# Kernel tuning notes

Hardware: AMD Instinct MI355X
Metric: run time of the kernel (lower is better)

Reference implementation:

```python
import jax, jax.numpy as jnp
import numpy as np

TOP_K = 2

def setup_inputs() -> dict:
    key = jax.random.key(0)
    k0, k1, k2, k3 = jax.random.split(key, 4)
    B, S, H, I, E = 2, 2048, 1024, 1408, 8
    hidden_states = jax.random.normal(k0, (B, S, H), dtype=jnp.float32)
    router_weight = jax.random.normal(k1, (E, H), dtype=jnp.float32) * 0.02
    gate_up_proj = jax.random.normal(k2, (E, 2 * I, H), dtype=jnp.float32) * 0.02
    down_proj = jax.random.normal(k3, (E, H, I), dtype=jnp.float32) * 0.02
    return {
        "hidden_states": hidden_states,
        "router_weight": router_weight,
        "gate_up_proj": gate_up_proj,
        "down_proj": down_proj,
    }

def reference(hidden_states, router_weight, gate_up_proj, down_proj):
    B, S, H = hidden_states.shape
    E = router_weight.shape[0]
    x = hidden_states.reshape(-1, H)                       # [T, H]
    T = x.shape[0]
    # Router: logits -> float32 softmax -> top-k (matches torch: topk on probs)
    logits = x @ router_weight.T                           # [T, E]
    probs = jax.nn.softmax(logits.astype(jnp.float32), axis=-1)
    topw, topi = jax.lax.top_k(probs, TOP_K)               # [T, K]
    topw = topw.astype(x.dtype)
    # Per-token combine weights over experts (zero for non-selected experts).
    combine = jnp.zeros((T, E), dtype=x.dtype)
    combine = combine.at[jnp.arange(T)[:, None], topi].set(topw)  # [T, E]
    # Dense grouped expert compute (same math as gather-GEMM-scatter loop:
    # tokens not routed to expert e get combine weight 0).
    gu = jnp.einsum('th,eoh->teo', x, gate_up_proj)        # [T, E, 2I]
    g, u = jnp.split(gu, 2, axis=-1)                       # [T, E, I] each
    h = jax.nn.silu(g) * u                                 # [T, E, I]
    y = jnp.einsum('tei,ehi->teh', h, down_proj)           # [T, E, H]
    out = jnp.einsum('teh,te->th', y, combine)             # [T, H]
    return out.reshape(B, S, H)
```

## Files before the change

kernel.cpp:

```cpp
#include <hip/hip_runtime.h>
#include <math.h>

#define NTOK 4096
#define HDIM 1024
#define NEXP 8
#define IDIM 1408
#define TWO_I 2816
#define TM 256
#define TK 64
#define NRB 40
#define ROWCAP (NRB * 256)

typedef _Float16 f16x8 __attribute__((ext_vector_type(8)));
typedef float f32x4 __attribute__((ext_vector_type(4)));

typedef __attribute__((address_space(1))) const unsigned int gu32;
typedef __attribute__((address_space(3))) unsigned int lu32;
__device__ __forceinline__ void async16(const void* g, void* l) {
  __builtin_amdgcn_global_load_lds((gu32*)g, (lu32*)l, 16, 0, 0);
}

__device__ __forceinline__ void seg_prefix(const int* __restrict__ counts, int* aof) {
  int o = 0; aof[0] = 0;
#pragma unroll
  for (int i = 0; i < 8; i++) { o += (counts[i] + 255) & ~255; aof[i + 1] = o; }
}

extern "C" __global__ void moe_init(int* counts, int* cursor, int* tok) {
  int i = blockIdx.x * 256 + threadIdx.x;
  if (i < NEXP) { counts[i] = 0; cursor[i] = 0; }
  if (i < ROWCAP) tok[i] = -1;
}

#define NG8 (NEXP * TWO_I * HDIM / 8)
#define ND8 (NEXP * HDIM * IDIM / 8)
extern "C" __global__ void moe_cvtw(const float* __restrict__ gup, const float* __restrict__ dp,
                                    _Float16* __restrict__ guph, _Float16* __restrict__ dph) {
  int i = blockIdx.x * 256 + threadIdx.x;
  const float4* s; uint4* d; size_t idx;
  if (i < NG8) { s = (const float4*)gup; d = (uint4*)guph; idx = i; }
  else if (i < NG8 + ND8) { s = (const float4*)dp; d = (uint4*)dph; idx = i - NG8; }
  else return;
  float4 a = s[idx * 2], b = s[idx * 2 + 1];
  union { _Float16 h[8]; uint4 u; } p;
  p.h[0] = (_Float16)a.x; p.h[1] = (_Float16)a.y; p.h[2] = (_Float16)a.z; p.h[3] = (_Float16)a.w;
  p.h[4] = (_Float16)b.x; p.h[5] = (_Float16)b.y; p.h[6] = (_Float16)b.z; p.h[7] = (_Float16)b.w;
  d[idx] = p.u;
}

extern "C" __global__ void moe_router(const float* __restrict__ x,
                                      const float* __restrict__ rw,
                                      int* __restrict__ topi,
                                      float* __restrict__ topw,
                                      _Float16* __restrict__ xh) {
  int w = threadIdx.x >> 6, lane = threadIdx.x & 63;
  int t = blockIdx.x * 4 + w;
  const float4* xp = (const float4*)(x + (size_t)t * HDIM);
  const float4* rp = (const float4*)rw;
  float acc[NEXP];
#pragma unroll
  for (int e = 0; e < NEXP; e++) acc[e] = 0.f;
#pragma unroll
  for (int i = 0; i < HDIM / 256; i++) {
    float4 xv = xp[i * 64 + lane];
    union { _Float16 h[4]; uint2 u; } pk;
    pk.h[0] = (_Float16)xv.x; pk.h[1] = (_Float16)xv.y;
    pk.h[2] = (_Float16)xv.z; pk.h[3] = (_Float16)xv.w;
    *(uint2*)(xh + (size_t)t * HDIM + i * 256 + lane * 4) = pk.u;
#pragma unroll
    for (int e = 0; e < NEXP; e++) {
      float4 rv = rp[e * 256 + i * 64 + lane];
      acc[e] += xv.x * rv.x + xv.y * rv.y + xv.z * rv.z + xv.w * rv.w;
    }
  }
#pragma unroll
  for (int e = 0; e < NEXP; e++) {
#pragma unroll
    for (int off = 32; off > 0; off >>= 1) acc[e] += __shfl_down(acc[e], off);
  }
  if (lane == 0) {
    float m = acc[0];
    for (int e = 1; e < NEXP; e++) m = fmaxf(m, acc[e]);
    float p[NEXP], s = 0.f;
    for (int e = 0; e < NEXP; e++) { p[e] = __expf(acc[e] - m); s += p[e]; }
    float inv = 1.f / s;
    int i0 = 0; float b0 = p[0];
    for (int e = 1; e < NEXP; e++) if (p[e] > b0) { b0 = p[e]; i0 = e; }
    int i1 = -1; float b1 = -1.f;
    for (int e = 0; e < NEXP; e++) if (e != i0 && p[e] > b1) { b1 = p[e]; i1 = e; }
    topi[t * 2] = i0; topi[t * 2 + 1] = i1;
    topw[t * 2] = b0 * inv; topw[t * 2 + 1] = b1 * inv;
  }
}

extern "C" __global__ void moe_count(const int* __restrict__ topi, int* __restrict__ counts) {
  __shared__ int cnt[NEXP];
  if (threadIdx.x < NEXP) cnt[threadIdx.x] = 0;
  __syncthreads();
  int t = blockIdx.x * 256 + threadIdx.x;
  atomicAdd(&cnt[topi[t * 2]], 1);
  atomicAdd(&cnt[topi[t * 2 + 1]], 1);
  __syncthreads();
  if (threadIdx.x < NEXP) atomicAdd(&counts[threadIdx.x], cnt[threadIdx.x]);
}

extern "C" __global__ void moe_scatter(const int* __restrict__ topi, const float* __restrict__ topw,
                                       const int* __restrict__ counts, int* __restrict__ cursor,
                                       int* __restrict__ tok, float* __restrict__ wrow,
                                       int* __restrict__ rows) {
  __shared__ int cnt[NEXP];
  __shared__ int base[NEXP];
  int aof[9]; seg_prefix(counts, aof);
  int tid = threadIdx.x;
  if (tid < NEXP) cnt[tid] = 0;
  __syncthreads();
  int t = blockIdx.x * 256 + tid;
  int e0 = topi[t * 2], e1 = topi[t * 2 + 1];
  int r0 = atomicAdd(&cnt[e0], 1);
  int r1 = atomicAdd(&cnt[e1], 1);
  __syncthreads();
  if (tid < NEXP) base[tid] = atomicAdd(&cursor[tid], cnt[tid]);
  __syncthreads();
  int row0 = aof[e0] + base[e0] + r0;
  int row1 = aof[e1] + base[e1] + r1;
  tok[row0] = t; wrow[row0] = topw[t * 2];     rows[t * 2]     = row0;
  tok[row1] = t; wrow[row1] = topw[t * 2 + 1]; rows[t * 2 + 1] = row1;
}


#define WAITVM(n) asm volatile("s_waitcnt vmcnt(" #n ")" ::: "memory")
#define BAR() __builtin_amdgcn_s_barrier()
#define PRIO(x) __builtin_amdgcn_s_setprio(x)

#define LDV(off) (*(const f16x8*)((const char*)smem + (uint32_t)(off)))

#define RD_A(grp, BO) { \
  _Pragma("unroll") for (int m_ = 0; m_ < 4; m_++) { \
    va[m_][0] = LDV(sA0 + (BO) + ((grp)*4 + m_)*2048); \
    va[m_][1] = LDV(sA1 + (BO) + ((grp)*4 + m_)*2048); } }

#define RD_B(VB, nb, BO) { \
  _Pragma("unroll") for (int n_ = 0; n_ < 2; n_++) { \
    VB[n_][0] = LDV(sB0 + (BO) + ((nb)*2 + n_)*2048); \
    VB[n_][1] = LDV(sB1 + (BO) + ((nb)*2 + n_)*2048); } }

#define MM(qa, qb, VB) { \
  _Pragma("unroll") for (int k_ = 0; k_ < 2; k_++) \
  _Pragma("unroll") for (int m_ = 0; m_ < 4; m_++) \
  _Pragma("unroll") for (int n_ = 0; n_ < 2; n_++) \
    acc[(qa)*4 + m_][(qb)*2 + n_] = __builtin_amdgcn_mfma_f32_16x16x32_f16( \
        va[m_][k_], VB[n_][k_], acc[(qa)*4 + m_][(qb)*2 + n_], 0, 0, 0); }

#define STG4(P, bf, r0, kt) { \
  async16(P[0][0] + (kt)*TK, smem + ((bf)*4 + (r0))*8192 + wv*512); \
  async16(P[0][1] + (kt)*TK, smem + ((bf)*4 + (r0))*8192 + 4096 + wv*512); \
  async16(P[1][0] + (kt)*TK, smem + ((bf)*4 + (r0) + 1)*8192 + wv*512); \
  async16(P[1][1] + (kt)*TK, smem + ((bf)*4 + (r0) + 1)*8192 + 4096 + wv*512); }
#define STAGE_A(bf, kt) STG4(pA, bf, 0, kt)
#define STAGE_B(bf, kt) STG4(pB, bf, 2, kt)

#define GEMM_CORE(NIT) { \
  STAGE_B(0, 0); STAGE_A(0, 0); \
  STAGE_B(1, 1); STAGE_A(1, 1); \
  WAITVM(8); BAR(); \
  _Pragma("unroll 1") \
  for (int it = 0; it < (NIT); ++it) { \
    const int nl = (it + 1 < (NIT)); \
    const int kt2 = 2*it + 2, kt3 = 2*it + 3; \
     RD_B(vb0, 0, 0); RD_A(0, 0); BAR(); PRIO(1); MM(0,0,vb0); PRIO(0); BAR(); \
     RD_B(vb1, 1, 0); BAR(); PRIO(1); MM(0,1,vb1); PRIO(0); BAR(); \
     RD_A(1, 0); if (nl) STAGE_B(0, kt2); BAR(); PRIO(1); MM(1,0,vb0); PRIO(0); BAR(); \
     if (nl) { STAGE_A(0, kt2); } PRIO(1); MM(1,1,vb1); PRIO(0); \
              if (nl) { WAITVM(8); } else { WAITVM(0); } BAR(); \
     RD_B(vb0, 0, 65536); RD_A(0, 65536); BAR(); PRIO(1); MM(0,0,vb0); PRIO(0); BAR(); \
     RD_B(vb1, 1, 65536); BAR(); PRIO(1); MM(0,1,vb1); PRIO(0); BAR(); \
     RD_A(1, 65536); if (nl) STAGE_B(1, kt3); BAR(); PRIO(1); MM(1,0,vb0); PRIO(0); BAR(); \
     if (nl) { STAGE_A(1, kt3); } PRIO(1); MM(1,1,vb1); PRIO(0); \
              if (nl) { WAITVM(8); } BAR(); \
  } \
  asm volatile("" ::: "memory"); }

#define GEMM_SETUP() \
  const int tid = threadIdx.x; \
  const int lane = tid & 63, wv = tid >> 6; \
  const int wm = wv >> 2, wn = wv & 3; \
  const int quad = lane >> 4, l15 = lane & 15; \
  const int srow = tid >> 3; \
  const int kc = ((tid & 7) ^ (srow & 7)) << 3; \
  const uint32_t c0 = (uint32_t)((quad * 16) ^ ((l15 & 7) << 4)); \
  const uint32_t c1 = c0 ^ 64; \
  const uint32_t sA0 = wm * 16384 + l15 * 128 + c0; \
  const uint32_t sA1 = wm * 16384 + l15 * 128 + c1; \
  const uint32_t sB0 = (2 + (wn >> 1)) * 16384 + ((wn & 1) * 64 + l15) * 128 + c0; \
  const uint32_t sB1 = (2 + (wn >> 1)) * 16384 + ((wn & 1) * 64 + l15) * 128 + c1; \
  f32x4 acc[8][4]; \
  _Pragma("unroll") for (int m = 0; m < 8; m++) \
  _Pragma("unroll") for (int n = 0; n < 4; n++) acc[m][n] = (f32x4){0.f, 0.f, 0.f, 0.f}; \
  f16x8 va[4][2], vb0[2][2], vb1[2][2];

extern "C" __global__ __launch_bounds__(512, 2) void moe_gemm1(
    const _Float16* __restrict__ xh, const _Float16* __restrict__ guph,
    const int* __restrict__ counts, const int* __restrict__ tok,
    _Float16* __restrict__ hbuf) {
  __shared__ __align__(128) _Float16 smem[65536];
  int aof[9]; seg_prefix(counts, aof);
  const int fid = blockIdx.x;
  const int g = fid & 7, t7 = fid >> 3;
  const int j = t7 / 5, r5 = t7 - j * 5;
  const int rb = g + 8 * r5;
  const int row0 = rb * TM;
  if (row0 >= aof[8]) return;
  int e = 0;
#pragma unroll
  for (int i = 0; i < 8; i++) if (row0 >= aof[i]) e = i;

  GEMM_SETUP();

  const _Float16* pA[2][2]; const _Float16* pB[2][2];
#pragma unroll
  for (int h = 0; h < 2; h++)
#pragma unroll
    for (int q = 0; q < 2; q++) {
      int tk = tok[row0 + h * 128 + q * 64 + srow];
      tk = tk < 0 ? 0 : tk;
      pA[h][q] = xh + (size_t)tk * HDIM + kc;
    }
  const _Float16* eb = guph + (size_t)e * TWO_I * HDIM;
#pragma unroll
  for (int q = 0; q < 2; q++) {
    pB[0][q] = eb + (size_t)(j * 128 + q * 64 + srow) * HDIM + kc;
    pB[1][q] = eb + (size_t)(IDIM + j * 128 + q * 64 + srow) * HDIM + kc;
  }

  GEMM_CORE(HDIM / (2 * TK))

  if (wn >= 2) {
#pragma unroll
    for (int mf = 0; mf < 8; mf++)
#pragma unroll
      for (int nf = 0; nf < 4; nf++)
#pragma unroll
        for (int r2 = 0; r2 < 4; r2++)
          smem[(wm * 128 + mf * 16 + quad * 4 + r2) * 132 + (wn - 2) * 64 + nf * 16 + l15] =
              (_Float16)acc[mf][nf][r2];
  }
  __syncthreads();
  if (wn < 2) {
#pragma unroll
    for (int mf = 0; mf < 8; mf++) {
#pragma unroll
      for (int r2 = 0; r2 < 4; r2++) {
        const int rl = wm * 128 + mf * 16 + quad * 4 + r2;
        _Float16* orow = hbuf + (size_t)(row0 + rl) * IDIM + j * 128 + wn * 64;
#pragma unroll
        for (int nf = 0; nf < 4; nf++) {
          float gg = acc[mf][nf][r2];
          float uu = (float)smem[rl * 132 + wn * 64 + nf * 16 + l15];
          float hh = gg / (1.f + __expf(-gg)) * uu;
          orow[nf * 16 + l15] = (_Float16)hh;
        }
      }
    }
  }
}

extern "C" __global__ __launch_bounds__(512, 2) void moe_gemm2(
    const _Float16* __restrict__ hbuf, const _Float16* __restrict__ dph,
    const int* __restrict__ counts, const float* __restrict__ wrow,
    _Float16* __restrict__ yh) {
  __shared__ __align__(128) _Float16 smem[65536];
  int aof[9]; seg_prefix(counts, aof);
  const int fid = blockIdx.x;
  const int g = fid & 7, t7 = fid >> 3;
  const int cb = t7 / 5, r5 = t7 - cb * 5;
  const int rb = g + 8 * r5;
  const int row0 = rb * TM;
  if (row0 >= aof[8]) return;
  int e = 0;
#pragma unroll
  for (int i = 0; i < 8; i++) if (row0 >= aof[i]) e = i;

  GEMM_SETUP();

  const _Float16* pA[2][2]; const _Float16* pB[2][2];
#pragma unroll
  for (int h = 0; h < 2; h++)
#pragma unroll
    for (int q = 0; q < 2; q++)
      pA[h][q] = hbuf + (size_t)(row0 + h * 128 + q * 64 + srow) * IDIM + kc;
  const _Float16* eb = dph + (size_t)e * HDIM * IDIM;
#pragma unroll
  for (int h = 0; h < 2; h++)
#pragma unroll
    for (int q = 0; q < 2; q++)
      pB[h][q] = eb + (size_t)(cb * 256 + h * 128 + q * 64 + srow) * IDIM + kc;

  GEMM_CORE(IDIM / (2 * TK))

#pragma unroll
  for (int mf = 0; mf < 8; mf++) {
#pragma unroll
    for (int r2 = 0; r2 < 4; r2++) {
      const int row = row0 + wm * 128 + mf * 16 + quad * 4 + r2;
      const float wgt = wrow[row];
      _Float16* orow = yh + (size_t)row * HDIM + cb * 256 + wn * 64;
#pragma unroll
      for (int nf = 0; nf < 4; nf++)
        orow[nf * 16 + l15] = (_Float16)(acc[mf][nf][r2] * wgt);
    }
  }
}

extern "C" __global__ void moe_combine(const _Float16* __restrict__ yh,
                                       const int* __restrict__ rows,
                                       float* __restrict__ out) {
  int i = blockIdx.x * 256 + threadIdx.x;
  int t = i >> 7, c8 = i & 127;
  int rA = rows[t * 2], rB = rows[t * 2 + 1];
  union { uint4 u; _Float16 h[8]; } pa, pb;
  pa.u = ((const uint4*)(yh + (size_t)rA * HDIM))[c8];
  pb.u = ((const uint4*)(yh + (size_t)rB * HDIM))[c8];
  float4 o0, o1;
  o0.x = (float)pa.h[0] + (float)pb.h[0]; o0.y = (float)pa.h[1] + (float)pb.h[1];
  o0.z = (float)pa.h[2] + (float)pb.h[2]; o0.w = (float)pa.h[3] + (float)pb.h[3];
  o1.x = (float)pa.h[4] + (float)pb.h[4]; o1.y = (float)pa.h[5] + (float)pb.h[5];
  o1.z = (float)pa.h[6] + (float)pb.h[6]; o1.w = (float)pa.h[7] + (float)pb.h[7];
  ((float4*)out)[(size_t)i * 2] = o0;
  ((float4*)out)[(size_t)i * 2 + 1] = o1;
}

extern "C" void kernel_launch(void* const* d_in, const int* in_sizes, int n_in,
                              void* d_out, int out_size, void* d_ws, size_t ws_size,
                              hipStream_t stream) {
  const float* x   = (const float*)d_in[0];
  const float* rw  = (const float*)d_in[1];
  const float* gup = (const float*)d_in[2];
  const float* dp  = (const float*)d_in[3];
  float* out = (float*)d_out;

  char* ws = (char*)d_ws;
  int*   counts = (int*)ws;
  int*   cursor = (int*)(ws + 64);
  int*   topi   = (int*)(ws + 4096);
  float* topw   = (float*)(ws + 36864);
  int*   tok    = (int*)(ws + 69632);
  float* wrow   = (float*)(ws + 110592);
  int*   rows   = (int*)(ws + 151552);
  _Float16* xh   = (_Float16*)(ws + 184320);
  _Float16* guph = (_Float16*)(ws + 8572928);
  _Float16* dph  = (_Float16*)(ws + 54710272);
  _Float16* hbuf = (_Float16*)(ws + 77778944);
  _Float16* yh   = (_Float16*)(ws + 8572928);

  moe_init<<<(ROWCAP + 255) / 256, 256, 0, stream>>>(counts, cursor, tok);
  moe_router<<<NTOK / 4, 256, 0, stream>>>(x, rw, topi, topw, xh);
  moe_count<<<NTOK / 256, 256, 0, stream>>>(topi, counts);
  moe_scatter<<<NTOK / 256, 256, 0, stream>>>(topi, topw, counts, cursor, tok, wrow, rows);
  moe_cvtw<<<(NG8 + ND8 + 255) / 256, 256, 0, stream>>>(gup, dp, guph, dph);
  moe_gemm1<<<8 * 11 * 5, 512, 0, stream>>>(xh, guph, counts, tok, hbuf);
  moe_gemm2<<<8 * 4 * 5, 512, 0, stream>>>(hbuf, dph, counts, wrow, yh);
  moe_combine<<<NTOK * HDIM / 8 / 256, 256, 0, stream>>>(yh, rows, out);
}
```

Before: 329.3 us.

## Simplify GEMM main loop to one LDS read phase and full MFMA block per k-tile

Replaces the four-quadrant interleaved schedule (partial A/B fragment reads, MFMA quarters, and barriers between each) with a simpler loop per K tile. Each iteration reads all A and B fragments, waits on LDS, issues one barrier, stages the tile two steps ahead, then runs all 64 MFMAs. This cuts barrier count and scheduling overhead, but holds more fragment registers at once (va[8][2], vb[4][2]). It also loses the overlap between LDS reads and MFMA work, which may expose LDS latency or hurt occupancy under the 512x2 launch bounds.

```diff
diff --git a/kernel.cpp b/kernel.cpp
--- a/kernel.cpp
+++ b/kernel.cpp
@@ -131,52 +131,47 @@
 #define WAITVM(n) asm volatile("s_waitcnt vmcnt(" #n ")" ::: "memory")
 #define BAR() __builtin_amdgcn_s_barrier()
 #define PRIO(x) __builtin_amdgcn_s_setprio(x)
+#define SCHEDB() __builtin_amdgcn_sched_barrier(0)
 
 #define LDV(off) (*(const f16x8*)((const char*)smem + (uint32_t)(off)))
 
-#define RD_A(grp, BO) { \
-  _Pragma("unroll") for (int m_ = 0; m_ < 4; m_++) { \
-    va[m_][0] = LDV(sA0 + (BO) + ((grp)*4 + m_)*2048); \
-    va[m_][1] = LDV(sA1 + (BO) + ((grp)*4 + m_)*2048); } }
-
-#define RD_B(VB, nb, BO) { \
-  _Pragma("unroll") for (int n_ = 0; n_ < 2; n_++) { \
-    VB[n_][0] = LDV(sB0 + (BO) + ((nb)*2 + n_)*2048); \
-    VB[n_][1] = LDV(sB1 + (BO) + ((nb)*2 + n_)*2048); } }
-
-#define MM(qa, qb, VB) { \
+#define RD_ALL(BO) { \
+  _Pragma("unroll") for (int m_ = 0; m_ < 8; m_++) { \
+    va[m_][0] = LDV(sA0 + (BO) + m_*2048); \
+    va[m_][1] = LDV(sA1 + (BO) + m_*2048); } \
+  _Pragma("unroll") for (int n_ = 0; n_ < 4; n_++) { \
+    vb[n_][0] = LDV(sB0 + (BO) + n_*2048); \
+    vb[n_][1] = LDV(sB1 + (BO) + n_*2048); } }
+
+#define MM_ALL() { \
   _Pragma("unroll") for (int k_ = 0; k_ < 2; k_++) \
-  _Pragma("unroll") for (int m_ = 0; m_ < 4; m_++) \
-  _Pragma("unroll") for (int n_ = 0; n_ < 2; n_++) \
-    acc[(qa)*4 + m_][(qb)*2 + n_] = __builtin_amdgcn_mfma_f32_16x16x32_f16( \
-        va[m_][k_], VB[n_][k_], acc[(qa)*4 + m_][(qb)*2 + n_], 0, 0, 0); }
+  _Pragma("unroll") for (int m_ = 0; m_ < 8; m_++) \
+  _Pragma("unroll") for (int n_ = 0; n_ < 4; n_++) \
+    acc[m_][n_] = __builtin_amdgcn_mfma_f32_16x16x32_f16( \
+        va[m_][k_], vb[n_][k_], acc[m_][n_], 0, 0, 0); }
 
 #define STG4(P, bf, r0, kt) { \
   async16(P[0][0] + (kt)*TK, smem + ((bf)*4 + (r0))*8192 + wv*512); \
   async16(P[0][1] + (kt)*TK, smem + ((bf)*4 + (r0))*8192 + 4096 + wv*512); \
   async16(P[1][0] + (kt)*TK, smem + ((bf)*4 + (r0) + 1)*8192 + wv*512); \
   async16(P[1][1] + (kt)*TK, smem + ((bf)*4 + (r0) + 1)*8192 + 4096 + wv*512); }
-#define STAGE_A(bf, kt) STG4(pA, bf, 0, kt)
-#define STAGE_B(bf, kt) STG4(pB, bf, 2, kt)
+#define STAGE_T(bf, kt) { STG4(pB, bf, 2, kt); STG4(pA, bf, 0, kt); }
 
 #define GEMM_CORE(NIT) { \
-  STAGE_B(0, 0); STAGE_A(0, 0); \
-  STAGE_B(1, 1); STAGE_A(1, 1); \
+  STAGE_T(0, 0); STAGE_T(1, 1); \
   WAITVM(8); BAR(); \
   _Pragma("unroll 1") \
-  for (int it = 0; it < (NIT); ++it) { \
-    const int nl = (it + 1 < (NIT)); \
-    const int kt2 = 2*it + 2, kt3 = 2*it + 3; \
-     RD_B(vb0, 0, 0); RD_A(0, 0); BAR(); PRIO(1); MM(0,0,vb0); PRIO(0); BAR(); \
-     RD_B(vb1, 1, 0); BAR(); PRIO(1); MM(0,1,vb1); PRIO(0); BAR(); \
-     RD_A(1, 0); if (nl) STAGE_B(0, kt2); BAR(); PRIO(1); MM(1,0,vb0); PRIO(0); BAR(); \
-     if (nl) { STAGE_A(0, kt2); } PRIO(1); MM(1,1,vb1); PRIO(0); \
-              if (nl) { WAITVM(8); } else { WAITVM(0); } BAR(); \
-     RD_B(vb0, 0, 65536); RD_A(0, 65536); BAR(); PRIO(1); MM(0,0,vb0); PRIO(0); BAR(); \
-     RD_B(vb1, 1, 65536); BAR(); PRIO(1); MM(0,1,vb1); PRIO(0); BAR(); \
-     RD_A(1, 65536); if (nl) STAGE_B(1, kt3); BAR(); PRIO(1); MM(1,0,vb0); PRIO(0); BAR(); \
-     if (nl) { STAGE_A(1, kt3); } PRIO(1); MM(1,1,vb1); PRIO(0); \
-              if (nl) { WAITVM(8); } BAR(); \
+  for (int kt = 0; kt < (NIT); ++kt) { \
+    const uint32_t BO = (kt & 1) ? 65536u : 0u; \
+    RD_ALL(BO); \
+    asm volatile("s_waitcnt lgkmcnt(0)" ::: "memory"); \
+    SCHEDB(); \
+    BAR(); \
+    SCHEDB(); \
+    if (kt + 2 < (NIT)) { STAGE_T((kt & 1), kt + 2); } \
+    PRIO(1); MM_ALL(); PRIO(0); \
+    if (kt + 2 < (NIT)) { WAITVM(8); } else { WAITVM(0); } \
+    BAR(); \
   } \
   asm volatile("" ::: "memory"); }
 
@@ -196,7 +191,7 @@
   f32x4 acc[8][4]; \
   _Pragma("unroll") for (int m = 0; m < 8; m++) \
   _Pragma("unroll") for (int n = 0; n < 4; n++) acc[m][n] = (f32x4){0.f, 0.f, 0.f, 0.f}; \
-  f16x8 va[4][2], vb0[2][2], vb1[2][2];
+  f16x8 va[8][2], vb[4][2];
 
 extern "C" __global__ __launch_bounds__(512, 2) void moe_gemm1(
     const _Float16* __restrict__ xh, const _Float16* __restrict__ guph,
@@ -232,7 +227,7 @@
     pB[1][q] = eb + (size_t)(IDIM + j * 128 + q * 64 + srow) * HDIM + kc;
   }
 
-  GEMM_CORE(HDIM / (2 * TK))
+  GEMM_CORE(HDIM / TK)
 
   if (wn >= 2) {
 #pragma unroll
@@ -295,7 +290,7 @@
     for (int q = 0; q < 2; q++)
       pB[h][q] = eb + (size_t)(cb * 256 + h * 128 + q * 64 + srow) * IDIM + kc;
 
-  GEMM_CORE(IDIM / (2 * TK))
+  GEMM_CORE(IDIM / TK)
 
 #pragma unroll
   for (int mf = 0; mf < 8; mf++) {
```

After: 335.8 us. No clear change (+2.0%).

## Fuse router with weight conversion and count, overlap down-proj cast with GEMM1, retile GEMM2

Applied to the files above, without the earlier changes.

Router, expert counting and the gate_up fp32->fp16 conversion now run in one launch, with the counting done by per-token global atomics. The down_proj conversion runs as extra blocks inside the GEMM1 launch, so it overlaps with that GEMM. GEMM2 moves to 128x128 tiles with 256 threads and a simpler double-buffered loop, which raises block count and occupancy. The cost is more contention on the global atomics and extra blocks competing with GEMM1 for compute units.

```diff
diff --git a/kernel.cpp b/kernel.cpp
--- a/kernel.cpp
+++ b/kernel.cpp
@@ -11,6 +11,11 @@
 #define NRB 40
 #define ROWCAP (NRB * 256)
 
+#define RT_BLKS 1024
+#define CVG_BLKS 2048
+#define G1_BLKS 440
+#define CVD_BLKS 256
+
 typedef _Float16 f16x8 __attribute__((ext_vector_type(8)));
 typedef float f32x4 __attribute__((ext_vector_type(4)));
 
@@ -26,21 +31,7 @@
   for (int i = 0; i < 8; i++) { o += (counts[i] + 255) & ~255; aof[i + 1] = o; }
 }
 
-extern "C" __global__ void moe_init(int* counts, int* cursor, int* tok) {
-  int i = blockIdx.x * 256 + threadIdx.x;
-  if (i < NEXP) { counts[i] = 0; cursor[i] = 0; }
-  if (i < ROWCAP) tok[i] = -1;
-}
-
-#define NG8 (NEXP * TWO_I * HDIM / 8)
-#define ND8 (NEXP * HDIM * IDIM / 8)
-extern "C" __global__ void moe_cvtw(const float* __restrict__ gup, const float* __restrict__ dp,
-                                    _Float16* __restrict__ guph, _Float16* __restrict__ dph) {
-  int i = blockIdx.x * 256 + threadIdx.x;
-  const float4* s; uint4* d; size_t idx;
-  if (i < NG8) { s = (const float4*)gup; d = (uint4*)guph; idx = i; }
-  else if (i < NG8 + ND8) { s = (const float4*)dp; d = (uint4*)dph; idx = i - NG8; }
-  else return;
+__device__ __forceinline__ void cvt8(const float4* __restrict__ s, uint4* __restrict__ d, size_t idx) {
   float4 a = s[idx * 2], b = s[idx * 2 + 1];
   union { _Float16 h[8]; uint4 u; } p;
   p.h[0] = (_Float16)a.x; p.h[1] = (_Float16)a.y; p.h[2] = (_Float16)a.z; p.h[3] = (_Float16)a.w;
@@ -48,11 +39,29 @@
   d[idx] = p.u;
 }
 
-extern "C" __global__ void moe_router(const float* __restrict__ x,
-                                      const float* __restrict__ rw,
-                                      int* __restrict__ topi,
-                                      float* __restrict__ topw,
-                                      _Float16* __restrict__ xh) {
+extern "C" __global__ void moe_init(int* counts, int* cursor, int* tok) {
+  int i = blockIdx.x * 256 + threadIdx.x;
+  if (i < NEXP) { counts[i] = 0; cursor[i] = 0; }
+  if (i < ROWCAP) tok[i] = -1;
+}
+
+#define NG8 (NEXP * TWO_I * HDIM / 8)
+#define ND8 (NEXP * HDIM * IDIM / 8)
+
+extern "C" __global__ void moe_rcv(const float* __restrict__ x,
+                                   const float* __restrict__ rw,
+                                   int* __restrict__ topi,
+                                   float* __restrict__ topw,
+                                   _Float16* __restrict__ xh,
+                                   int* __restrict__ counts,
+                                   const float* __restrict__ gup,
+                                   _Float16* __restrict__ guph) {
+  if (blockIdx.x >= RT_BLKS) {
+    size_t idx = (size_t)(blockIdx.x - RT_BLKS) * 256 + threadIdx.x;
+    const float4* s = (const float4*)gup; uint4* d = (uint4*)guph;
+    for (; idx < NG8; idx += (size_t)CVG_BLKS * 256) cvt8(s, d, idx);
+    return;
+  }
   int w = threadIdx.x >> 6, lane = threadIdx.x & 63;
   int t = blockIdx.x * 4 + w;
   const float4* xp = (const float4*)(x + (size_t)t * HDIM);
@@ -90,18 +99,9 @@
     for (int e = 0; e < NEXP; e++) if (e != i0 && p[e] > b1) { b1 = p[e]; i1 = e; }
     topi[t * 2] = i0; topi[t * 2 + 1] = i1;
     topw[t * 2] = b0 * inv; topw[t * 2 + 1] = b1 * inv;
-  }
-}
-
-extern "C" __global__ void moe_count(const int* __restrict__ topi, int* __restrict__ counts) {
-  __shared__ int cnt[NEXP];
-  if (threadIdx.x < NEXP) cnt[threadIdx.x] = 0;
-  __syncthreads();
-  int t = blockIdx.x * 256 + threadIdx.x;
-  atomicAdd(&cnt[topi[t * 2]], 1);
-  atomicAdd(&cnt[topi[t * 2 + 1]], 1);
-  __syncthreads();
-  if (threadIdx.x < NEXP) atomicAdd(&counts[threadIdx.x], cnt[threadIdx.x]);
+    atomicAdd(&counts[i0], 1);
+    atomicAdd(&counts[i1], 1);
+  }
 }
 
 extern "C" __global__ void moe_scatter(const int* __restrict__ topi, const float* __restrict__ topw,
@@ -127,7 +127,6 @@
   tok[row1] = t; wrow[row1] = topw[t * 2 + 1]; rows[t * 2 + 1] = row1;
 }
 
-
 #define WAITVM(n) asm volatile("s_waitcnt vmcnt(" #n ")" ::: "memory")
 #define BAR() __builtin_amdgcn_s_barrier()
 #define PRIO(x) __builtin_amdgcn_s_setprio(x)
@@ -181,7 +180,6 @@
   asm volatile("" ::: "memory"); }
 
 #define GEMM_SETUP() \
-  const int tid = threadIdx.x; \
   const int lane = tid & 63, wv = tid >> 6; \
   const int wm = wv >> 2, wn = wv & 3; \
   const int quad = lane >> 4, l15 = lane & 15; \
@@ -198,13 +196,21 @@
   _Pragma("unroll") for (int n = 0; n < 4; n++) acc[m][n] = (f32x4){0.f, 0.f, 0.f, 0.f}; \
   f16x8 va[4][2], vb0[2][2], vb1[2][2];
 
-extern "C" __global__ __launch_bounds__(512, 2) void moe_gemm1(
+extern "C" __global__ __launch_bounds__(512, 2) void moe_gemm1cd(
     const _Float16* __restrict__ xh, const _Float16* __restrict__ guph,
     const int* __restrict__ counts, const int* __restrict__ tok,
-    _Float16* __restrict__ hbuf) {
+    _Float16* __restrict__ hbuf,
+    const float* __restrict__ dp, _Float16* __restrict__ dph) {
   __shared__ __align__(128) _Float16 smem[65536];
+  const int tid = threadIdx.x;
+  const int fid = blockIdx.x;
+  if (fid >= G1_BLKS) {
+    size_t idx = (size_t)(fid - G1_BLKS) * 512 + tid;
+    const float4* s = (const float4*)dp; uint4* d = (uint4*)dph;
+    for (; idx < ND8; idx += (size_t)CVD_BLKS * 512) cvt8(s, d, idx);
+    return;
+  }
   int aof[9]; seg_prefix(counts, aof);
-  const int fid = blockIdx.x;
   const int g = fid & 7, t7 = fid >> 3;
   const int j = t7 / 5, r5 = t7 - j * 5;
   const int rb = g + 8 * r5;
@@ -264,49 +270,98 @@
   }
 }
 
-extern "C" __global__ __launch_bounds__(512, 2) void moe_gemm2(
+extern "C" __global__ __launch_bounds__(256, 2) void moe_gemm2(
     const _Float16* __restrict__ hbuf, const _Float16* __restrict__ dph,
     const int* __restrict__ counts, const float* __restrict__ wrow,
     _Float16* __restrict__ yh) {
-  __shared__ __align__(128) _Float16 smem[65536];
+  __shared__ __align__(128) _Float16 smem[32768];
   int aof[9]; seg_prefix(counts, aof);
   const int fid = blockIdx.x;
   const int g = fid & 7, t7 = fid >> 3;
-  const int cb = t7 / 5, r5 = t7 - cb * 5;
-  const int rb = g + 8 * r5;
-  const int row0 = rb * TM;
+  const int cb = t7 / 10, r10 = t7 - cb * 10;
+  const int rb = g + 8 * r10;
+  const int row0 = rb * 128;
   if (row0 >= aof[8]) return;
   int e = 0;
 #pragma unroll
   for (int i = 0; i < 8; i++) if (row0 >= aof[i]) e = i;
 
-  GEMM_SETUP();
-
-  const _Float16* pA[2][2]; const _Float16* pB[2][2];
-#pragma unroll
-  for (int h = 0; h < 2; h++)
-#pragma unroll
-    for (int q = 0; q < 2; q++)
-      pA[h][q] = hbuf + (size_t)(row0 + h * 128 + q * 64 + srow) * IDIM + kc;
+  const int tid = threadIdx.x;
+  const int lane = tid & 63, wv = tid >> 6;
+  const int wm = wv >> 1, wn = wv & 1;
+  const int quad = lane >> 4, l15 = lane & 15;
+  const int kc = ((tid & 7) ^ ((tid >> 3) & 7)) << 3;
+  const uint32_t c0 = (uint32_t)((quad * 16) ^ ((l15 & 7) << 4));
+  const uint32_t c1 = c0 ^ 64;
+  const uint32_t sA_0 = (uint32_t)((wm * 64 + l15) * 128) + c0;
+  const uint32_t sA_1 = (uint32_t)((wm * 64 + l15) * 128) + c1;
+  const uint32_t sB_0 = 16384u + (uint32_t)((wn * 64 + l15) * 128) + c0;
+  const uint32_t sB_1 = 16384u + (uint32_t)((wn * 64 + l15) * 128) + c1;
+
+  f32x4 acc2[4][4];
+#pragma unroll
+  for (int m = 0; m < 4; m++)
+#pragma unroll
+    for (int n = 0; n < 4; n++) acc2[m][n] = (f32x4){0.f, 0.f, 0.f, 0.f};
+  f16x8 va2[4][2], vb2[4][2];
+
+  const _Float16* pA2[4]; const _Float16* pB2[4];
   const _Float16* eb = dph + (size_t)e * HDIM * IDIM;
 #pragma unroll
-  for (int h = 0; h < 2; h++)
-#pragma unroll
-    for (int q = 0; q < 2; q++)
-      pB[h][q] = eb + (size_t)(cb * 256 + h * 128 + q * 64 + srow) * IDIM + kc;
-
-  GEMM_CORE(IDIM / (2 * TK))
-
-#pragma unroll
-  for (int mf = 0; mf < 8; mf++) {
+  for (int c = 0; c < 4; c++) {
+    pA2[c] = hbuf + (size_t)(row0 + c * 32 + (tid >> 3)) * IDIM + kc;
+    pB2[c] = eb + (size_t)(cb * 128 + c * 32 + (tid >> 3)) * IDIM + kc;
+  }
+
+#define STG2(bf, kt) { \
+  _Pragma("unroll") for (int c_ = 0; c_ < 4; c_++) { \
+    async16(pA2[c_] + (kt)*TK, smem + (bf)*16384 + c_*2048 + tid*8); \
+    async16(pB2[c_] + (kt)*TK, smem + (bf)*16384 + 8192 + c_*2048 + tid*8); } }
+
+  const int NIT2 = IDIM / TK;
+  STG2(0, 0); STG2(1, 1);
+  WAITVM(8); BAR();
+#pragma unroll 1
+  for (int kt = 0; kt < NIT2; ++kt) {
+    const uint32_t BO = (kt & 1) ? 32768u : 0u;
+#pragma unroll
+    for (int m_ = 0; m_ < 4; m_++) {
+      va2[m_][0] = LDV(sA_0 + BO + m_ * 2048);
+      va2[m_][1] = LDV(sA_1 + BO + m_ * 2048);
+    }
+#pragma unroll
+    for (int n_ = 0; n_ < 4; n_++) {
+      vb2[n_][0] = LDV(sB_0 + BO + n_ * 2048);
+      vb2[n_][1] = LDV(sB_1 + BO + n_ * 2048);
+    }
+    asm volatile("s_waitcnt lgkmcnt(0)" ::: "memory");
+    BAR();
+    if (kt + 2 < NIT2) { STG2((kt & 1), kt + 2); }
+    PRIO(1);
+#pragma unroll
+    for (int k_ = 0; k_ < 2; k_++)
+#pragma unroll
+      for (int m_ = 0; m_ < 4; m_++)
+#pragma unroll
+        for (int n_ = 0; n_ < 4; n_++)
+          acc2[m_][n_] = __builtin_amdgcn_mfma_f32_16x16x32_f16(
+              va2[m_][k_], vb2[n_][k_], acc2[m_][n_], 0, 0, 0);
+    PRIO(0);
+    if (kt + 2 < NIT2) { WAITVM(8); } else { WAITVM(0); }
+    BAR();
+  }
+#undef STG2
+
+#pragma unroll
+  for (int mf = 0; mf < 4; mf++) {
 #pragma unroll
     for (int r2 = 0; r2 < 4; r2++) {
-      const int row = row0 + wm * 128 + mf * 16 + quad * 4 + r2;
+      const int row = row0 + wm * 64 + mf * 16 + quad * 4 + r2;
       const float wgt = wrow[row];
-      _Float16* orow = yh + (size_t)row * HDIM + cb * 256 + wn * 64;
+      _Float16* orow = yh + (size_t)row * HDIM + cb * 128 + wn * 64;
 #pragma unroll
       for (int nf = 0; nf < 4; nf++)
-        orow[nf * 16 + l15] = (_Float16)(acc[mf][nf][r2] * wgt);
+        orow[nf * 16 + l15] = (_Float16)(acc2[mf][nf][r2] * wgt);
     }
   }
 }
@@ -353,11 +408,9 @@
   _Float16* yh   = (_Float16*)(ws + 8572928);
 
   moe_init<<<(ROWCAP + 255) / 256, 256, 0, stream>>>(counts, cursor, tok);
-  moe_router<<<NTOK / 4, 256, 0, stream>>>(x, rw, topi, topw, xh);
-  moe_count<<<NTOK / 256, 256, 0, stream>>>(topi, counts);
+  moe_rcv<<<RT_BLKS + CVG_BLKS, 256, 0, stream>>>(x, rw, topi, topw, xh, counts, gup, guph);
   moe_scatter<<<NTOK / 256, 256, 0, stream>>>(topi, topw, counts, cursor, tok, wrow, rows);
-  moe_cvtw<<<(NG8 + ND8 + 255) / 256, 256, 0, stream>>>(gup, dp, guph, dph);
-  moe_gemm1<<<8 * 11 * 5, 512, 0, stream>>>(xh, guph, counts, tok, hbuf);
-  moe_gemm2<<<8 * 4 * 5, 512, 0, stream>>>(hbuf, dph, counts, wrow, yh);
+  moe_gemm1cd<<<G1_BLKS + CVD_BLKS, 512, 0, stream>>>(xh, guph, counts, tok, hbuf, dp, dph);
+  moe_gemm2<<<8 * 8 * 10, 256, 0, stream>>>(hbuf, dph, counts, wrow, yh);
   moe_combine<<<NTOK * HDIM / 8 / 256, 256, 0, stream>>>(yh, rows, out);
 }
```

Result: slower. 386.4 us (+17.3%).
